# Kernel tuning notes

Measured on AMD Instinct MI355X. Metric: run time of the kernel, lower is better.

Reference implementation:

```python
import jax, jax.numpy as jnp
import numpy as np

N_NODES = 50000
N_EDGES = 600000
IN_DIM = 128
EDGE_DIM = 64
OUT_DIM = 128
AVG_D_LOG = 2.5
EPS = 1e-5  # std epsilon used by PNA aggregate_std
POST_IN = (4 * 3 + 1) * IN_DIM  # (n_aggr*n_scalers + 1) * in_dim = 1664


def setup_inputs() -> dict:
    key = jax.random.key(0)
    ks = jax.random.split(key, 10)
    node_feat = jax.random.normal(ks[0], (N_NODES, IN_DIM), dtype=jnp.float32)
    edge_feat = jax.random.normal(ks[1], (N_EDGES, EDGE_DIM), dtype=jnp.float32)
    src = jax.random.randint(ks[2], (N_EDGES,), 0, N_NODES, dtype=jnp.int32)
    dst = jax.random.randint(ks[3], (N_EDGES,), 0, N_NODES, dtype=jnp.int32)
    pre_in = 2 * IN_DIM + EDGE_DIM  # 320
    W_pre = jax.random.normal(ks[4], (pre_in, IN_DIM), dtype=jnp.float32) / np.sqrt(pre_in)
    b_pre = jnp.zeros((IN_DIM,), dtype=jnp.float32)
    W_post1 = jax.random.normal(ks[5], (POST_IN, OUT_DIM), dtype=jnp.float32) / np.sqrt(POST_IN)
    b_post1 = jnp.zeros((OUT_DIM,), dtype=jnp.float32)
    W_post2 = jax.random.normal(ks[6], (OUT_DIM, OUT_DIM), dtype=jnp.float32) / np.sqrt(OUT_DIM)
    b_post2 = jnp.zeros((OUT_DIM,), dtype=jnp.float32)
    return {"node_feat": node_feat, "edge_feat": edge_feat, "src": src, "dst": dst,
            "W_pre": W_pre, "b_pre": b_pre, "W_post1": W_post1, "b_post1": b_post1,
            "W_post2": W_post2, "b_post2": b_post2}


def reference(node_feat, edge_feat, src, dst, W_pre, b_pre, W_post1, b_post1, W_post2, b_post2):
    N = node_feat.shape[0]
    # pretrans_edges: concat(src feat, dst feat, edge feat) -> MLP (1 layer + relu)
    z2 = jnp.concatenate([node_feat[src], node_feat[dst], edge_feat], axis=-1)  # [E, 320]
    e = jax.nn.relu(z2 @ W_pre + b_pre)  # [E, in_dim] edge messages

    # segmented multi-aggregator reduce at destination nodes
    deg = jax.ops.segment_sum(jnp.ones((e.shape[0],), e.dtype), dst, num_segments=N)  # [N]
    safe_deg = jnp.maximum(deg, 1.0)[:, None]
    s = jax.ops.segment_sum(e, dst, num_segments=N)
    mean = s / safe_deg
    mean_sq = jax.ops.segment_sum(e * e, dst, num_segments=N) / safe_deg
    var = jax.nn.relu(mean_sq - mean * mean)
    std = jnp.sqrt(var + EPS)
    mx = jax.ops.segment_max(e, dst, num_segments=N)
    mn = jax.ops.segment_min(e, dst, num_segments=N)
    has_edges = (deg > 0)[:, None]
    mean = jnp.where(has_edges, mean, 0.0)
    mx = jnp.where(has_edges, mx, 0.0)
    mn = jnp.where(has_edges, mn, 0.0)
    std = jnp.where(has_edges, std, 0.0)
    agg = jnp.concatenate([mean, mx, mn, std], axis=-1)  # [N, 4*in_dim]

    # scalers: identity, amplification, attenuation
    logd = jnp.log(deg + 1.0)[:, None]
    amp = agg * (logd / AVG_D_LOG)
    att = agg * jnp.where(deg[:, None] > 0, AVG_D_LOG / jnp.maximum(logd, EPS), 0.0)
    h_agg = jnp.concatenate([agg, amp, att], axis=-1)  # [N, 12*in_dim]

    # posttrans: concat(h, aggregated) -> 2-layer MLP, then residual
    h = jnp.concatenate([node_feat, h_agg], axis=-1)  # [N, 13*in_dim]
    h = jax.nn.relu(h @ W_post1 + b_post1)
    h = h @ W_post2 + b_post2
    return h + node_feat  # residual (in_dim == out_dim)
```

## Files before the change

kernel.cpp:

```cpp
#include <hip/hip_runtime.h>
#include <hip/hip_bf16.h>
#include <math.h>

#define N_NODES 50000
#define N_EDGES 600000
#define EG 3750
#define SCAN_NB 196

typedef __attribute__((ext_vector_type(8))) short short8v;
typedef __attribute__((ext_vector_type(4))) short short4v;
typedef __attribute__((ext_vector_type(4))) float f32x4;
typedef __attribute__((ext_vector_type(4))) float float4v;

#define FLT_BIG 3.402823466e38f

__device__ __forceinline__ short f2bf(float f) {
  unsigned int u = __float_as_uint(f);
  u = (u + 0x7FFFu + ((u >> 16) & 1u)) >> 16;
  return (short)u;
}
__device__ __forceinline__ float bf2f(unsigned short s) {
  return __uint_as_float(((unsigned int)s) << 16);
}

__global__ void conv_w_kernel(const float* __restrict__ Wpre, const float* __restrict__ Wp1,
                              const float* __restrict__ Wp2, short* __restrict__ WuvT,
                              short* __restrict__ WeT, short* __restrict__ Wp1T,
                              short* __restrict__ Wp2T, int* __restrict__ deg) {
  int idx = blockIdx.x * 256 + threadIdx.x;
  if (idx < 50048) deg[idx] = 0;
  if (idx < 32768) {
    int c = idx >> 7, k = idx & 127;
    WuvT[idx] = f2bf(Wpre[(k + ((c >> 7) << 7)) * 128 + (c & 127)]);
  } else if (idx < 40960) {
    int o = idx - 32768, n = o >> 6, k = o & 63;
    WeT[o] = f2bf(Wpre[(256 + k) * 128 + n]);
  } else if (idx < 253952) {
    int o = idx - 40960, n = o / 1664, k = o % 1664;
    Wp1T[o] = f2bf(Wp1[k * 128 + n]);
  } else if (idx < 270336) {
    int o = idx - 253952, n = o >> 7, k = o & 127;
    Wp2T[o] = f2bf(Wp2[k * 128 + n]);
  }
}

__global__ void deg_kernel(const int* __restrict__ dst, int* __restrict__ deg) {
  int i = blockIdx.x * blockDim.x + threadIdx.x;
  int stride = gridDim.x * blockDim.x;
  for (; i < N_EDGES; i += stride) atomicAdd(deg + dst[i], 1);
}

__global__ __launch_bounds__(256) void scan1_kernel(const int* __restrict__ deg,
                                                    int* __restrict__ blockSums) {
  __shared__ int red[256];
  int b = blockIdx.x, t = threadIdx.x;
  int n = b * 256 + t;
  red[t] = (n < N_NODES) ? deg[n] : 0;
  __syncthreads();
  for (int off = 128; off > 0; off >>= 1) {
    if (t < off) red[t] += red[t + off];
    __syncthreads();
  }
  if (t == 0) blockSums[b] = red[0];
}

__global__ __launch_bounds__(256) void scan2_kernel(const int* __restrict__ blockSums,
                                                    int* __restrict__ blockOffs) {
  __shared__ int sh[256];
  int t = threadIdx.x;
  int v = (t < SCAN_NB) ? blockSums[t] : 0;
  sh[t] = v;
  __syncthreads();
  for (int off = 1; off < 256; off <<= 1) {
    int u = (t >= off) ? sh[t - off] : 0;
    __syncthreads();
    sh[t] += u;
    __syncthreads();
  }
  if (t < SCAN_NB) blockOffs[t] = sh[t] - v;
}

__global__ __launch_bounds__(256) void scan3_kernel(const int* __restrict__ deg,
                                                    const int* __restrict__ blockOffs,
                                                    int* __restrict__ cursor,
                                                    int* __restrict__ rowStart) {
  __shared__ int sh[256];
  int b = blockIdx.x, t = threadIdx.x;
  int n = b * 256 + t;
  int v = (n < N_NODES) ? deg[n] : 0;
  sh[t] = v;
  __syncthreads();
  for (int off = 1; off < 256; off <<= 1) {
    int u = (t >= off) ? sh[t - off] : 0;
    __syncthreads();
    sh[t] += u;
    __syncthreads();
  }
  int ex = blockOffs[b] + sh[t] - v;
  if (n < N_NODES) { cursor[n] = ex; rowStart[n] = ex; }
  if (n == N_NODES) rowStart[N_NODES] = N_EDGES;
}

__global__ void scatter_kernel(const int* __restrict__ src, const int* __restrict__ dst,
                               int* __restrict__ cursor, const int* __restrict__ rowStart,
                               int4* __restrict__ eid, int* __restrict__ blockA) {
  int i0 = blockIdx.x * blockDim.x + threadIdx.x;
  int stride = gridDim.x * blockDim.x;
  for (int i = i0; i < N_EDGES; i += stride) {
    int d = dst[i];
    int pos = atomicAdd(cursor + d, 1);
    eid[pos] = make_int4(i, src[i], d, 0);
  }
  for (int j = N_EDGES + i0; j < N_EDGES + 64; j += stride)
    eid[j] = make_int4(0, 0, 0, 0);
  for (int b = i0; b <= EG; b += stride) {
    int tgt = (int)((long)b * N_EDGES / EG);
    int lo = 0, hi = N_NODES;
    while (lo < hi) { int mid = (lo + hi) >> 1; if (rowStart[mid] < tgt) lo = mid + 1; else hi = mid; }
    blockA[b] = rowStart[lo];
  }
}

__global__ __launch_bounds__(256) void uv_kernel(const float* __restrict__ nf,
                                                 const short* __restrict__ WuvT,
                                                 short* __restrict__ UV) {
  __shared__ short A[64][136];
  int t = threadIdx.x;
  int lane = t & 63, w = t >> 6;
  int r15 = lane & 15, g = lane >> 4;
  int nb = blockIdx.x * 64;

#pragma unroll
  for (int i = 0; i < 8; i++) {
    int u = t + 256 * i, row = u >> 5, q = u & 31;
    int gn = min(nb + row, N_NODES - 1);
    float4v a = *(const float4v*)(nf + (size_t)gn * 128 + q * 4);
    short4v s;
    s[0] = f2bf(a[0]); s[1] = f2bf(a[1]); s[2] = f2bf(a[2]); s[3] = f2bf(a[3]);
    *(short4v*)(&A[row][q * 4]) = s;
  }
  __syncthreads();

  f32x4 acc[4][4];
#pragma unroll
  for (int m = 0; m < 4; m++)
#pragma unroll
    for (int j = 0; j < 4; j++) acc[m][j] = (f32x4){0.f, 0.f, 0.f, 0.f};

#pragma unroll
  for (int ks = 0; ks < 4; ks++) {
    short8v af[4];
#pragma unroll
    for (int m = 0; m < 4; m++) af[m] = *(const short8v*)(&A[m * 16 + r15][ks * 32 + 8 * g]);
#pragma unroll
    for (int j = 0; j < 4; j++) {
      short8v bf = *(const short8v*)(WuvT + (size_t)((4 * w + j) * 16 + r15) * 128 + ks * 32 + 8 * g);
#pragma unroll
      for (int m = 0; m < 4; m++)
        acc[m][j] = __builtin_amdgcn_mfma_f32_16x16x32_bf16(af[m], bf, acc[m][j], 0, 0, 0);
    }
  }

#pragma unroll
  for (int m = 0; m < 4; m++)
#pragma unroll
    for (int j = 0; j < 4; j++)
#pragma unroll
      for (int r = 0; r < 4; r++) {
        int node = nb + m * 16 + 4 * g + r;
        if (node < N_NODES)
          UV[(size_t)node * 256 + (4 * w + j) * 16 + r15] = f2bf(acc[m][j][r]);
      }
}

__global__ __launch_bounds__(256, 6) void edge_kernel(
    const int4* __restrict__ eid, const int* __restrict__ blockA,
    const float* __restrict__ edge_feat, const float* __restrict__ b_pre,
    const short* __restrict__ UV, const short* __restrict__ WeT,
    float* __restrict__ sum, float* __restrict__ sq,
    float* __restrict__ mx, float* __restrict__ mn) {
  __shared__ short A[32][72];
  __shared__ float E[32][132];
  __shared__ int srcL[2][32], dstL[2][32];

  int t = threadIdx.x;
  int lane = t & 63, w = t >> 6;
  int r15 = lane & 15, g = lane >> 4;

  short8v bfr[2][2];
#pragma unroll
  for (int ks = 0; ks < 2; ks++)
#pragma unroll
    for (int j = 0; j < 2; j++)
      bfr[ks][j] = *(const short8v*)(WeT + (size_t)((2 * w + j) * 16 + r15) * 64 + ks * 32 + 8 * g);

  int c = t & 127, half = t >> 7;
  int cd = t & 63, wrow = t >> 6;
  float bp0 = b_pre[2 * cd], bp1 = b_pre[2 * cd + 1];

  const unsigned short* UVu = (const unsigned short*)UV;
  int A0 = blockA[blockIdx.x], A1 = blockA[blockIdx.x + 1];
  if (A0 >= A1) return;

  float4v ge[2];
  auto LOADE = [&](int e0c) {
#pragma unroll
    for (int i = 0; i < 2; i++) {
      int u = t + 256 * i, e = u >> 4, q = u & 15;
      int pe = eid[min(e0c + e, N_EDGES + 63)].x;
      ge[i] = *(const float4v*)(edge_feat + (size_t)pe * 64 + q * 4);
    }
  };
  auto WRITE_A = [&]() {
#pragma unroll
    for (int i = 0; i < 2; i++) {
      int u = t + 256 * i, e = u >> 4, q = u & 15;
      short4v s4;
      s4[0] = f2bf(ge[i][0]); s4[1] = f2bf(ge[i][1]);
      s4[2] = f2bf(ge[i][2]); s4[3] = f2bf(ge[i][3]);
      *(short4v*)(&A[e][q * 4]) = s4;
    }
  };
  int nsrc = 0, ndst = 0;
  auto IDXLOAD = [&](int e0c) {
    if (t < 32) {
      int4 v = eid[min(e0c + t, N_EDGES + 63)];
      nsrc = v.y; ndst = v.z;
    }
  };

  LOADE(A0);
  IDXLOAD(A0);
  if (t < 32) { srcL[0][t] = nsrc; dstL[0][t] = ndst; }
  WRITE_A();
  IDXLOAD(A0 + 32);
  __syncthreads();

  float a0 = (half == 0) ? 0.f : -FLT_BIG;
  float a1 = (half == 0) ? 0.f : FLT_BIG;
  int prevd = -1;

  int p = 0;
  for (int e0 = A0; e0 < A1; e0 += 32) {
    int cnt = min(32, A1 - e0);
    unsigned int upf[8], vpf[8];
#pragma unroll
    for (int i = 0; i < 8; i++) {
      int rr = min(wrow + 4 * i, cnt - 1);
      int sr = srcL[p][rr], dr = dstL[p][rr];
      upf[i] = *(const unsigned int*)(UVu + (size_t)sr * 256 + 2 * cd);
      vpf[i] = *(const unsigned int*)(UVu + (size_t)dr * 256 + 128 + 2 * cd);
    }
    LOADE(e0 + 32);

    f32x4 acc[2][2];
#pragma unroll
    for (int m = 0; m < 2; m++)
#pragma unroll
      for (int j = 0; j < 2; j++) acc[m][j] = (f32x4){0.f, 0.f, 0.f, 0.f};
#pragma unroll
    for (int m = 0; m < 2; m++)
#pragma unroll
      for (int ks = 0; ks < 2; ks++) {
        short8v af = *(const short8v*)(&A[m * 16 + r15][ks * 32 + 8 * g]);
        acc[m][0] = __builtin_amdgcn_mfma_f32_16x16x32_bf16(af, bfr[ks][0], acc[m][0], 0, 0, 0);
        acc[m][1] = __builtin_amdgcn_mfma_f32_16x16x32_bf16(af, bfr[ks][1], acc[m][1], 0, 0, 0);
      }
#pragma unroll
    for (int m = 0; m < 2; m++)
#pragma unroll
      for (int j = 0; j < 2; j++)
#pragma unroll
        for (int r = 0; r < 4; r++)
          E[m * 16 + 4 * g + r][(2 * w + j) * 16 + r15] = acc[m][j][r];
    __syncthreads();

#pragma unroll
    for (int i = 0; i < 8; i++) {
      int r = wrow + 4 * i;
      float u0 = bf2f((unsigned short)(upf[i] & 0xFFFFu));
      float u1 = bf2f((unsigned short)(upf[i] >> 16));
      float v0 = bf2f((unsigned short)(vpf[i] & 0xFFFFu));
      float v1 = bf2f((unsigned short)(vpf[i] >> 16));
      E[r][2 * cd] = fmaxf(u0 + v0 + E[r][2 * cd] + bp0, 0.f);
      E[r][2 * cd + 1] = fmaxf(u1 + v1 + E[r][2 * cd + 1] + bp1, 0.f);
    }
    __syncthreads();

    {
      int l = lane & 31;
      int dl_ = dstL[p][l];
      int dp_ = (l == 0) ? prevd : dstL[p][l - 1];
      unsigned int bm = (unsigned int)__ballot(dl_ != dp_);
#pragma unroll
      for (int r = 0; r < 32; r++) {
        if (r < cnt) {
          if ((bm >> r) & 1u) {
            int tgt = (r == 0) ? prevd : dstL[p][r - 1];
            if (tgt >= 0) {
              size_t o = (size_t)tgt * 128 + c;
              if (half == 0) { sum[o] = a0; sq[o] = a1; }
              else { mx[o] = a0; mn[o] = a1; }
            }
            if (half == 0) { a0 = 0.f; a1 = 0.f; }
            else { a0 = -FLT_BIG; a1 = FLT_BIG; }
          }
          float e = E[r][c];
          if (half == 0) { a0 += e; a1 += e * e; }
          else { a0 = fmaxf(a0, e); a1 = fminf(a1, e); }
        }
      }
      prevd = dstL[p][cnt - 1];
    }
    WRITE_A();
    if (t < 32) { srcL[p ^ 1][t] = nsrc; dstL[p ^ 1][t] = ndst; }
    IDXLOAD(e0 + 64);
    __syncthreads();
    p ^= 1;
  }
  if (prevd >= 0) {
    size_t o = (size_t)prevd * 128 + c;
    if (half == 0) { sum[o] = a0; sq[o] = a1; }
    else { mx[o] = a0; mn[o] = a1; }
  }
}

__global__ __launch_bounds__(512, 4) void post_kernel(
    const float* __restrict__ node_feat, const int* __restrict__ deg,
    const float* __restrict__ sum, const float* __restrict__ sq,
    const float* __restrict__ mxp, const float* __restrict__ mnp,
    const short* __restrict__ Wp1T, const short* __restrict__ Wp2T,
    const float* __restrict__ b1, const float* __restrict__ b2,
    float* __restrict__ out) {
  __shared__ short Ab[2][64][64];
  __shared__ short T[64][136];
  __shared__ float scalL[64][4];
  int t = threadIdx.x;
  int lane = t & 63, w = t >> 6;
  int r15 = lane & 15, g = lane >> 4;
  int nb = blockIdx.x * 64;

  if (t < 64) {
    int n = min(nb + t, N_NODES - 1);
    float dg = (float)deg[n];
    scalL[t][0] = 1.f / fmaxf(dg, 1.f);
    float logd = logf(dg + 1.f);
    scalL[t][1] = logd * 0.4f;
    scalL[t][2] = (dg > 0.f) ? 2.5f / fmaxf(logd, 1e-5f) : 0.f;
    scalL[t][3] = (dg > 0.f) ? 1.f : 0.f;
  }
  float bb1v = b1[w * 16 + r15];

  int srow = t >> 3, s8 = t & 7;
  int sgn = min(nb + srow, N_NODES - 1);
  float4v ra, rb, qa, qb;

  auto PRE = [&](int c) {
    if (c < 2) {
      const float* np = node_feat + (size_t)sgn * 128 + c * 64 + s8 * 8;
      ra = *(const float4v*)np;
      rb = *(const float4v*)(np + 4);
    } else {
      size_t o = (size_t)sgn * 128 + (c & 1) * 64 + s8 * 8;
      int si = (c - 2) >> 1;
      if (si == 0) { ra = *(const float4v*)(sum + o); rb = *(const float4v*)(sum + o + 4); }
      else if (si == 1) { ra = *(const float4v*)(mxp + o); rb = *(const float4v*)(mxp + o + 4); }
      else if (si == 2) { ra = *(const float4v*)(mnp + o); rb = *(const float4v*)(mnp + o + 4); }
      else {
        ra = *(const float4v*)(sum + o); rb = *(const float4v*)(sum + o + 4);
        qa = *(const float4v*)(sq + o);  qb = *(const float4v*)(sq + o + 4);
      }
    }
  };
  auto WR = [&](int buf, int c) {
    short8v pk;
    if (c < 2) {
#pragma unroll
      for (int r = 0; r < 4; r++) { pk[r] = f2bf(ra[r]); pk[4 + r] = f2bf(rb[r]); }
    } else {
      int si = (c - 2) >> 1;
      float inv = scalL[srow][0];
      bool h = (scalL[srow][3] != 0.f);
      if (si == 0) {
#pragma unroll
        for (int r = 0; r < 4; r++) {
          pk[r] = f2bf(h ? ra[r] * inv : 0.f);
          pk[4 + r] = f2bf(h ? rb[r] * inv : 0.f);
        }
      } else if (si == 1) {
#pragma unroll
        for (int r = 0; r < 4; r++) {
          pk[r] = f2bf(h ? ra[r] : 0.f);
          pk[4 + r] = f2bf(h ? rb[r] : 0.f);
        }
      } else if (si == 2) {
#pragma unroll
        for (int r = 0; r < 4; r++) {
          pk[r] = f2bf(h ? ra[r] : 0.f);
          pk[4 + r] = f2bf(h ? rb[r] : 0.f);
        }
      } else {
#pragma unroll
        for (int r = 0; r < 4; r++) {
          float m0 = ra[r] * inv, m1 = rb[r] * inv;
          float s0 = sqrtf(fmaxf(qa[r] * inv - m0 * m0, 0.f) + 1e-5f);
          float s1 = sqrtf(fmaxf(qb[r] * inv - m1 * m1, 0.f) + 1e-5f);
          pk[r] = f2bf(h ? s0 : 0.f);
          pk[4 + r] = f2bf(h ? s1 : 0.f);
        }
      }
    }
    *(short8v*)(&Ab[buf][0][0] + srow * 64 + (s8 ^ (srow & 7)) * 8) = pk;
  };

  f32x4 accB[4], accC[4], accD[4];
#pragma unroll
  for (int m = 0; m < 4; m++) {
    accB[m] = (f32x4){0.f, 0.f, 0.f, 0.f};
    accC[m] = (f32x4){0.f, 0.f, 0.f, 0.f};
    accD[m] = (f32x4){0.f, 0.f, 0.f, 0.f};
  }

  const short* wrp = Wp1T + (size_t)(w * 16 + r15) * 1664 + 8 * g;

  PRE(0);
  __syncthreads();
  WR(0, 0);
  __syncthreads();

  for (int c = 0; c < 10; c++) {
    int buf = c & 1;
    if (c < 9) PRE(c + 1);
    short8v bw0[3], bw1[3];
    if (c < 2) {
      bw0[0] = *(const short8v*)(wrp + c * 64);
      bw1[0] = *(const short8v*)(wrp + c * 64 + 32);
    } else {
      int ka = (c - 2) * 64;
      bw0[0] = *(const short8v*)(wrp + 128 + ka);
      bw0[1] = *(const short8v*)(wrp + 640 + ka);
      bw0[2] = *(const short8v*)(wrp + 1152 + ka);
      bw1[0] = *(const short8v*)(wrp + 128 + ka + 32);
      bw1[1] = *(const short8v*)(wrp + 640 + ka + 32);
      bw1[2] = *(const short8v*)(wrp + 1152 + ka + 32);
    }
    const short* base = &Ab[buf][0][0];
#pragma unroll
    for (int ks2 = 0; ks2 < 2; ks2++) {
      const short8v* bw = (ks2 == 0) ? bw0 : bw1;
      short8v af[4];
#pragma unroll
      for (int m = 0; m < 4; m++) {
        int row = m * 16 + r15;
        af[m] = *(const short8v*)(base + row * 64 + (((ks2 << 2) | g) ^ (row & 7)) * 8);
      }
      if (c < 2) {
#pragma unroll
        for (int m = 0; m < 4; m++)
          accB[m] = __builtin_amdgcn_mfma_f32_16x16x32_bf16(af[m], bw[0], accB[m], 0, 0, 0);
      } else {
#pragma unroll
        for (int m = 0; m < 4; m++) {
          accB[m] = __builtin_amdgcn_mfma_f32_16x16x32_bf16(af[m], bw[0], accB[m], 0, 0, 0);
          accC[m] = __builtin_amdgcn_mfma_f32_16x16x32_bf16(af[m], bw[1], accC[m], 0, 0, 0);
          accD[m] = __builtin_amdgcn_mfma_f32_16x16x32_bf16(af[m], bw[2], accD[m], 0, 0, 0);
        }
      }
    }
    if (c < 9) WR(buf ^ 1, c + 1);
    __syncthreads();
  }

#pragma unroll
  for (int m = 0; m < 4; m++)
#pragma unroll
    for (int r = 0; r < 4; r++) {
      int row = m * 16 + 4 * g + r;
      float v = accB[m][r] + scalL[row][1] * accC[m][r] + scalL[row][2] * accD[m][r] + bb1v;
      T[row][w * 16 + r15] = f2bf(fmaxf(v, 0.f));
    }
  __syncthreads();

  f32x4 acc2[4];
#pragma unroll
  for (int m = 0; m < 4; m++) acc2[m] = (f32x4){0.f, 0.f, 0.f, 0.f};
#pragma unroll
  for (int ks = 0; ks < 4; ks++) {
    short8v af2[4];
#pragma unroll
    for (int m = 0; m < 4; m++) af2[m] = *(const short8v*)(&T[m * 16 + r15][ks * 32 + 8 * g]);
    short8v b2f = *(const short8v*)(Wp2T + (size_t)(w * 16 + r15) * 128 + ks * 32 + 8 * g);
#pragma unroll
    for (int m = 0; m < 4; m++)
      acc2[m] = __builtin_amdgcn_mfma_f32_16x16x32_bf16(af2[m], b2f, acc2[m], 0, 0, 0);
  }

#pragma unroll
  for (int m = 0; m < 4; m++)
#pragma unroll
    for (int r = 0; r < 4; r++) {
      int row = m * 16 + 4 * g + r;
      int gn = nb + row;
      if (gn < N_NODES) {
        int col = w * 16 + r15;
        size_t o = (size_t)gn * 128 + col;
        out[o] = acc2[m][r] + b2[col] + node_feat[o];
      }
    }
}

extern "C" void kernel_launch(void* const* d_in, const int* in_sizes, int n_in,
                              void* d_out, int out_size, void* d_ws, size_t ws_size,
                              hipStream_t stream) {
  const float* node_feat = (const float*)d_in[0];
  const float* edge_feat = (const float*)d_in[1];
  const int* src = (const int*)d_in[2];
  const int* dst = (const int*)d_in[3];
  const float* W_pre = (const float*)d_in[4];
  const float* b_pre = (const float*)d_in[5];
  const float* W_post1 = (const float*)d_in[6];
  const float* b_post1 = (const float*)d_in[7];
  const float* W_post2 = (const float*)d_in[8];
  const float* b_post2 = (const float*)d_in[9];
  float* out = (float*)d_out;

  char* ws = (char*)d_ws;
  size_t P = (size_t)N_NODES * 128;
  float* sum = (float*)ws;
  float* sq = sum + P;
  float* mx = sq + P;
  float* mn = mx + P;
  int* deg = (int*)(mn + P);
  int* cursor = deg + 50048;
  int* rowStart = cursor + 50048;
  int* blockA = rowStart + 50052;
  int* blockSums = blockA + 3752;
  int* blockOffs = blockSums + 256;
  int4* eid = (int4*)(blockOffs + 256);
  short* UV = (short*)(eid + N_EDGES + 64);
  short* WuvT = UV + (size_t)50048 * 256;
  short* WeT = WuvT + 32768;
  short* Wp1T = WeT + 8192;
  short* Wp2T = Wp1T + 212992;
  size_t needed = (size_t)((char*)(Wp2T + 16384) - ws);
  if (ws_size < needed) return;

  conv_w_kernel<<<(270336 + 255) / 256, 256, 0, stream>>>(W_pre, W_post1, W_post2, WuvT, WeT,
                                                          Wp1T, Wp2T, deg);
  deg_kernel<<<1024, 256, 0, stream>>>(dst, deg);
  scan1_kernel<<<SCAN_NB, 256, 0, stream>>>(deg, blockSums);
  scan2_kernel<<<1, 256, 0, stream>>>(blockSums, blockOffs);
  scan3_kernel<<<SCAN_NB, 256, 0, stream>>>(deg, blockOffs, cursor, rowStart);
  scatter_kernel<<<1024, 256, 0, stream>>>(src, dst, cursor, rowStart, eid, blockA);
  uv_kernel<<<(N_NODES + 63) / 64, 256, 0, stream>>>(node_feat, WuvT, UV);
  edge_kernel<<<EG, 256, 0, stream>>>(eid, blockA, edge_feat, b_pre, UV, WeT, sum, sq, mx, mn);
  post_kernel<<<(N_NODES + 63) / 64, 512, 0, stream>>>(node_feat, deg, sum, sq, mx, mn, Wp1T,
                                                       Wp2T, b_post1, b_post2, out);
}
```

Baseline: 288.3 us.

## Merge scan stages and run UV GEMM alongside edge scatter in one launch

Folds the single-block block-sum scan into every block of the per-node scan, so each block redundantly rescans 196 partial sums and one launch disappears. Merges the UV node GEMM and the CSR scatter into one kernel with disjoint block ranges, so the independent work overlaps and a second launch disappears. Moves the b_pre bias into the V half of the UV precompute instead of adding it per edge. The bias is now added before bf16 rounding, which changes numerics slightly.

```diff
diff --git a/kernel.cpp b/kernel.cpp
--- a/kernel.cpp
+++ b/kernel.cpp
@@ -6,6 +6,7 @@
 #define N_EDGES 600000
 #define EG 3750
 #define SCAN_NB 196
+#define UV_NB 782
 
 typedef __attribute__((ext_vector_type(8))) short short8v;
 typedef __attribute__((ext_vector_type(4))) short short4v;
@@ -64,28 +65,22 @@
   if (t == 0) blockSums[b] = red[0];
 }
 
-__global__ __launch_bounds__(256) void scan2_kernel(const int* __restrict__ blockSums,
-                                                    int* __restrict__ blockOffs) {
-  __shared__ int sh[256];
-  int t = threadIdx.x;
-  int v = (t < SCAN_NB) ? blockSums[t] : 0;
-  sh[t] = v;
-  __syncthreads();
-  for (int off = 1; off < 256; off <<= 1) {
-    int u = (t >= off) ? sh[t - off] : 0;
-    __syncthreads();
-    sh[t] += u;
-    __syncthreads();
-  }
-  if (t < SCAN_NB) blockOffs[t] = sh[t] - v;
-}
-
-__global__ __launch_bounds__(256) void scan3_kernel(const int* __restrict__ deg,
-                                                    const int* __restrict__ blockOffs,
-                                                    int* __restrict__ cursor,
-                                                    int* __restrict__ rowStart) {
+__global__ __launch_bounds__(256) void scan23_kernel(const int* __restrict__ deg,
+                                                     const int* __restrict__ blockSums,
+                                                     int* __restrict__ cursor,
+                                                     int* __restrict__ rowStart) {
+  __shared__ int bs[256];
   __shared__ int sh[256];
   int b = blockIdx.x, t = threadIdx.x;
+  bs[t] = (t < SCAN_NB) ? blockSums[t] : 0;
+  __syncthreads();
+  for (int off = 1; off < 256; off <<= 1) {
+    int u = (t >= off) ? bs[t - off] : 0;
+    __syncthreads();
+    bs[t] += u;
+    __syncthreads();
+  }
+  int blockOff = (b == 0) ? 0 : bs[b - 1];
   int n = b * 256 + t;
   int v = (n < N_NODES) ? deg[n] : 0;
   sh[t] = v;
@@ -96,86 +91,89 @@
     sh[t] += u;
     __syncthreads();
   }
-  int ex = blockOffs[b] + sh[t] - v;
+  int ex = blockOff + sh[t] - v;
   if (n < N_NODES) { cursor[n] = ex; rowStart[n] = ex; }
   if (n == N_NODES) rowStart[N_NODES] = N_EDGES;
 }
 
-__global__ void scatter_kernel(const int* __restrict__ src, const int* __restrict__ dst,
-                               int* __restrict__ cursor, const int* __restrict__ rowStart,
-                               int4* __restrict__ eid, int* __restrict__ blockA) {
-  int i0 = blockIdx.x * blockDim.x + threadIdx.x;
-  int stride = gridDim.x * blockDim.x;
-  for (int i = i0; i < N_EDGES; i += stride) {
-    int d = dst[i];
-    int pos = atomicAdd(cursor + d, 1);
-    eid[pos] = make_int4(i, src[i], d, 0);
-  }
-  for (int j = N_EDGES + i0; j < N_EDGES + 64; j += stride)
-    eid[j] = make_int4(0, 0, 0, 0);
-  for (int b = i0; b <= EG; b += stride) {
-    int tgt = (int)((long)b * N_EDGES / EG);
-    int lo = 0, hi = N_NODES;
-    while (lo < hi) { int mid = (lo + hi) >> 1; if (rowStart[mid] < tgt) lo = mid + 1; else hi = mid; }
-    blockA[b] = rowStart[lo];
-  }
-}
-
-__global__ __launch_bounds__(256) void uv_kernel(const float* __restrict__ nf,
-                                                 const short* __restrict__ WuvT,
-                                                 short* __restrict__ UV) {
+__global__ __launch_bounds__(256) void scatter_uv_kernel(
+    const float* __restrict__ nf, const short* __restrict__ WuvT,
+    const float* __restrict__ b_pre, short* __restrict__ UV,
+    const int* __restrict__ src, const int* __restrict__ dst,
+    int* __restrict__ cursor, const int* __restrict__ rowStart,
+    int4* __restrict__ eid, int* __restrict__ blockA) {
   __shared__ short A[64][136];
   int t = threadIdx.x;
-  int lane = t & 63, w = t >> 6;
-  int r15 = lane & 15, g = lane >> 4;
-  int nb = blockIdx.x * 64;
-
-#pragma unroll
-  for (int i = 0; i < 8; i++) {
-    int u = t + 256 * i, row = u >> 5, q = u & 31;
-    int gn = min(nb + row, N_NODES - 1);
-    float4v a = *(const float4v*)(nf + (size_t)gn * 128 + q * 4);
-    short4v s;
-    s[0] = f2bf(a[0]); s[1] = f2bf(a[1]); s[2] = f2bf(a[2]); s[3] = f2bf(a[3]);
-    *(short4v*)(&A[row][q * 4]) = s;
-  }
-  __syncthreads();
-
-  f32x4 acc[4][4];
-#pragma unroll
-  for (int m = 0; m < 4; m++)
-#pragma unroll
-    for (int j = 0; j < 4; j++) acc[m][j] = (f32x4){0.f, 0.f, 0.f, 0.f};
-
-#pragma unroll
-  for (int ks = 0; ks < 4; ks++) {
-    short8v af[4];
-#pragma unroll
-    for (int m = 0; m < 4; m++) af[m] = *(const short8v*)(&A[m * 16 + r15][ks * 32 + 8 * g]);
+  if (blockIdx.x < UV_NB) {
+    int lane = t & 63, w = t >> 6;
+    int r15 = lane & 15, g = lane >> 4;
+    int nb = blockIdx.x * 64;
+#pragma unroll
+    for (int i = 0; i < 8; i++) {
+      int u = t + 256 * i, row = u >> 5, q = u & 31;
+      int gn = min(nb + row, N_NODES - 1);
+      float4v a = *(const float4v*)(nf + (size_t)gn * 128 + q * 4);
+      short4v s;
+      s[0] = f2bf(a[0]); s[1] = f2bf(a[1]); s[2] = f2bf(a[2]); s[3] = f2bf(a[3]);
+      *(short4v*)(&A[row][q * 4]) = s;
+    }
+    __syncthreads();
+
+    f32x4 acc[4][4];
+#pragma unroll
+    for (int m = 0; m < 4; m++)
+#pragma unroll
+      for (int j = 0; j < 4; j++) acc[m][j] = (f32x4){0.f, 0.f, 0.f, 0.f};
+
+#pragma unroll
+    for (int ks = 0; ks < 4; ks++) {
+      short8v af[4];
+#pragma unroll
+      for (int m = 0; m < 4; m++) af[m] = *(const short8v*)(&A[m * 16 + r15][ks * 32 + 8 * g]);
+#pragma unroll
+      for (int j = 0; j < 4; j++) {
+        short8v bf = *(const short8v*)(WuvT + (size_t)((4 * w + j) * 16 + r15) * 128 + ks * 32 + 8 * g);
+#pragma unroll
+        for (int m = 0; m < 4; m++)
+          acc[m][j] = __builtin_amdgcn_mfma_f32_16x16x32_bf16(af[m], bf, acc[m][j], 0, 0, 0);
+      }
+    }
+
 #pragma unroll
     for (int j = 0; j < 4; j++) {
-      short8v bf = *(const short8v*)(WuvT + (size_t)((4 * w + j) * 16 + r15) * 128 + ks * 32 + 8 * g);
+      int coln = (4 * w + j) * 16 + r15;
+      float bias = (coln >= 128) ? b_pre[coln - 128] : 0.f;
 #pragma unroll
       for (int m = 0; m < 4; m++)
-        acc[m][j] = __builtin_amdgcn_mfma_f32_16x16x32_bf16(af[m], bf, acc[m][j], 0, 0, 0);
-    }
-  }
-
-#pragma unroll
-  for (int m = 0; m < 4; m++)
-#pragma unroll
-    for (int j = 0; j < 4; j++)
-#pragma unroll
-      for (int r = 0; r < 4; r++) {
-        int node = nb + m * 16 + 4 * g + r;
-        if (node < N_NODES)
-          UV[(size_t)node * 256 + (4 * w + j) * 16 + r15] = f2bf(acc[m][j][r]);
-      }
+#pragma unroll
+        for (int r = 0; r < 4; r++) {
+          int node = nb + m * 16 + 4 * g + r;
+          if (node < N_NODES)
+            UV[(size_t)node * 256 + coln] = f2bf(acc[m][j][r] + bias);
+        }
+    }
+  } else {
+    int i0 = (blockIdx.x - UV_NB) * 256 + t;
+    int stride = 1024 * 256;
+    for (int i = i0; i < N_EDGES; i += stride) {
+      int d = dst[i];
+      int pos = atomicAdd(cursor + d, 1);
+      eid[pos] = make_int4(i, src[i], d, 0);
+    }
+    for (int j = N_EDGES + i0; j < N_EDGES + 64; j += stride)
+      eid[j] = make_int4(0, 0, 0, 0);
+    for (int b = i0; b <= EG; b += stride) {
+      int tgt = (int)((long)b * N_EDGES / EG);
+      int lo = 0, hi = N_NODES;
+      while (lo < hi) { int mid = (lo + hi) >> 1; if (rowStart[mid] < tgt) lo = mid + 1; else hi = mid; }
+      blockA[b] = rowStart[lo];
+    }
+  }
 }
 
 __global__ __launch_bounds__(256, 6) void edge_kernel(
     const int4* __restrict__ eid, const int* __restrict__ blockA,
-    const float* __restrict__ edge_feat, const float* __restrict__ b_pre,
+    const float* __restrict__ edge_feat,
     const short* __restrict__ UV, const short* __restrict__ WeT,
     float* __restrict__ sum, float* __restrict__ sq,
     float* __restrict__ mx, float* __restrict__ mn) {
@@ -196,7 +194,6 @@
 
   int c = t & 127, half = t >> 7;
   int cd = t & 63, wrow = t >> 6;
-  float bp0 = b_pre[2 * cd], bp1 = b_pre[2 * cd + 1];
 
   const unsigned short* UVu = (const unsigned short*)UV;
   int A0 = blockA[blockIdx.x], A1 = blockA[blockIdx.x + 1];
@@ -282,8 +279,8 @@
       float u1 = bf2f((unsigned short)(upf[i] >> 16));
       float v0 = bf2f((unsigned short)(vpf[i] & 0xFFFFu));
       float v1 = bf2f((unsigned short)(vpf[i] >> 16));
-      E[r][2 * cd] = fmaxf(u0 + v0 + E[r][2 * cd] + bp0, 0.f);
-      E[r][2 * cd + 1] = fmaxf(u1 + v1 + E[r][2 * cd + 1] + bp1, 0.f);
+      E[r][2 * cd] = fmaxf(u0 + v0 + E[r][2 * cd], 0.f);
+      E[r][2 * cd + 1] = fmaxf(u1 + v1 + E[r][2 * cd + 1], 0.f);
     }
     __syncthreads();
 
@@ -535,8 +532,8 @@
   int* rowStart = cursor + 50048;
   int* blockA = rowStart + 50052;
   int* blockSums = blockA + 3752;
-  int* blockOffs = blockSums + 256;
-  int4* eid = (int4*)(blockOffs + 256);
+  int* pad = blockSums + 256;
+  int4* eid = (int4*)(pad + 256);
   short* UV = (short*)(eid + N_EDGES + 64);
   short* WuvT = UV + (size_t)50048 * 256;
   short* WeT = WuvT + 32768;
@@ -549,11 +546,10 @@
                                                           Wp1T, Wp2T, deg);
   deg_kernel<<<1024, 256, 0, stream>>>(dst, deg);
   scan1_kernel<<<SCAN_NB, 256, 0, stream>>>(deg, blockSums);
-  scan2_kernel<<<1, 256, 0, stream>>>(blockSums, blockOffs);
-  scan3_kernel<<<SCAN_NB, 256, 0, stream>>>(deg, blockOffs, cursor, rowStart);
-  scatter_kernel<<<1024, 256, 0, stream>>>(src, dst, cursor, rowStart, eid, blockA);
-  uv_kernel<<<(N_NODES + 63) / 64, 256, 0, stream>>>(node_feat, WuvT, UV);
-  edge_kernel<<<EG, 256, 0, stream>>>(eid, blockA, edge_feat, b_pre, UV, WeT, sum, sq, mx, mn);
+  scan23_kernel<<<SCAN_NB, 256, 0, stream>>>(deg, blockSums, cursor, rowStart);
+  scatter_uv_kernel<<<UV_NB + 1024, 256, 0, stream>>>(node_feat, WuvT, b_pre, UV, src, dst,
+                                                      cursor, rowStart, eid, blockA);
+  edge_kernel<<<EG, 256, 0, stream>>>(eid, blockA, edge_feat, UV, WeT, sum, sq, mx, mn);
   post_kernel<<<(N_NODES + 63) / 64, 512, 0, stream>>>(node_feat, deg, sum, sq, mx, mn, Wp1T,
                                                        Wp2T, b_post1, b_post2, out);
 }
```

Result: slower. 305.0 us (+5.8%).
